# Optimization experiments

Hardware: AMD Instinct MI355X
Metric: run time of the kernel (lower is better)

The kernel has to match this reference:

```python
import jax, jax.numpy as jnp
import numpy as np

D_MODEL = 1024
D_FF = 4096
N_EXPERTS = 8
TOP_K = 2
BATCH, SEQ = 4, 1024


def setup_inputs() -> dict:
    key = jax.random.key(0)
    ks = jax.random.split(key, 5)
    x = jax.random.normal(ks[0], (BATCH, SEQ, D_MODEL), jnp.float32)
    Wr = jax.random.normal(ks[1], (D_MODEL, N_EXPERTS), jnp.float32) * (D_MODEL ** -0.5)
    W1 = jax.random.normal(ks[2], (N_EXPERTS, D_MODEL, D_FF), jnp.float32) * (D_MODEL ** -0.5)
    b1 = jnp.zeros((N_EXPERTS, D_FF), jnp.float32)
    W2 = jax.random.normal(ks[3], (N_EXPERTS, D_FF, D_MODEL), jnp.float32) * (D_FF ** -0.5)
    b2 = jnp.zeros((N_EXPERTS, D_MODEL), jnp.float32)
    return {"x": x, "Wr": Wr, "W1": W1, "b1": b1, "W2": W2, "b2": b2}


def reference(x, Wr, W1, b1, W2, b2):
    B, S, D = x.shape
    E = Wr.shape[1]
    xf = x.reshape(-1, D)                         # [T, D], T = B*S
    # Router: softmax over experts, pick top-k, renormalize gates over the k picks
    probs = jax.nn.softmax(xf @ Wr, axis=-1)      # [T, E]
    top_v, top_i = jax.lax.top_k(probs, TOP_K)    # [T, K]
    gates = top_v / jnp.sum(top_v, axis=-1, keepdims=True)
    # Combine weights per (token, expert): weight is gate if expert selected else 0
    cw = jnp.sum(gates[:, :, None] * jax.nn.one_hot(top_i, E, dtype=x.dtype), axis=1)  # [T, E]
    # Expert MLPs: loop over the small fixed expert count, weighted scatter-add combine
    out = jnp.zeros_like(xf)
    for e in range(E):
        h = jax.nn.relu(xf @ W1[e] + b1[e])       # [T, d_ff]
        y = h @ W2[e] + b2[e]                     # [T, D]
        out = out + cw[:, e:e + 1] * y
    return out.reshape(x.shape)
```

## Files before the change

kernel.cpp:

```cpp
#include <hip/hip_runtime.h>


#define T_TOK 4096
#define DMODEL 1024
#define DFF 4096
#define NE 8
#define CAP 9216

typedef __bf16 bf16x8 __attribute__((ext_vector_type(8)));
typedef float f32x4 __attribute__((ext_vector_type(4)));

__device__ __forceinline__ unsigned short f2bf(float f) {
    union { float f; unsigned u; } v; v.f = f;
    unsigned r = v.u + 0x7fffu + ((v.u >> 16) & 1u);
    return (unsigned short)(r >> 16);
}

__device__ __forceinline__ void gld16(const unsigned short* g, unsigned short* l) {
    __builtin_amdgcn_global_load_lds(
        (const __attribute__((address_space(1))) unsigned int*)g,
        (__attribute__((address_space(3))) unsigned int*)l, 16, 0, 0);
}

__global__ __launch_bounds__(256) void k_router(const float* __restrict__ x,
                                                const float* __restrict__ Wr,
                                                int* __restrict__ meta,
                                                int* __restrict__ tg_idx,
                                                float* __restrict__ tg_gate) {
    int wave = threadIdx.x >> 6, lane = threadIdx.x & 63;
    int t = blockIdx.x * 4 + wave;
    double acc[NE];
#pragma unroll
    for (int e = 0; e < NE; e++) acc[e] = 0.0;
    const float* xr = x + (size_t)t * DMODEL;
#pragma unroll 4
    for (int j = 0; j < 16; j++) {
        int k = j * 64 + lane;
        double xv = (double)xr[k];
        const float4* wr = (const float4*)(Wr + k * NE);
        float4 w0 = wr[0], w1 = wr[1];
        acc[0] += xv * (double)w0.x; acc[1] += xv * (double)w0.y;
        acc[2] += xv * (double)w0.z; acc[3] += xv * (double)w0.w;
        acc[4] += xv * (double)w1.x; acc[5] += xv * (double)w1.y;
        acc[6] += xv * (double)w1.z; acc[7] += xv * (double)w1.w;
    }
#pragma unroll
    for (int off = 32; off; off >>= 1)
#pragma unroll
        for (int e = 0; e < NE; e++) acc[e] += __shfl_xor(acc[e], off);
    if (lane == 0) {
        double v1 = -1e300, v2 = -1e300; int i1 = 0, i2 = 0;
#pragma unroll
        for (int e = 0; e < NE; e++) {
            double v = acc[e];
            if (v > v1) { v2 = v1; i2 = i1; v1 = v; i1 = e; }
            else if (v > v2) { v2 = v; i2 = e; }
        }
        double g1 = 1.0 / (1.0 + exp(v2 - v1));
        tg_idx[t * 2] = i1; tg_idx[t * 2 + 1] = i2;
        tg_gate[t * 2] = (float)g1; tg_gate[t * 2 + 1] = (float)(1.0 - g1);
        atomicAdd(&meta[i1], 1);
        atomicAdd(&meta[i2], 1);
    }
}

__global__ void k_scan(int* __restrict__ meta) {
    if (threadIdx.x == 0) {
        int acc = 0;
        for (int e = 0; e < NE; e++) {
            int a = (meta[e] + 127) & ~127;
            meta[16 + e] = a;
            meta[24 + e] = acc;
            acc += a;
        }
        meta[24 + NE] = acc;
        meta[33] = acc;
    }
}

__global__ __launch_bounds__(256) void k_build(const int* __restrict__ tg_idx,
                                               const float* __restrict__ tg_gate,
                                               int* __restrict__ meta,
                                               int* __restrict__ tos,
                                               float* __restrict__ gos,
                                               int* __restrict__ sot) {
    int t = blockIdx.x * 256 + threadIdx.x;
#pragma unroll
    for (int kk = 0; kk < 2; kk++) {
        int e = tg_idx[t * 2 + kk];
        int pos = atomicAdd(&meta[8 + e], 1);
        int slot = meta[24 + e] + pos;
        tos[slot] = t;
        gos[slot] = tg_gate[t * 2 + kk];
        sot[t * 2 + kk] = slot;
    }
}

__global__ __launch_bounds__(256) void k_gather(const float* __restrict__ x,
                                                const int* __restrict__ tos,
                                                const int* __restrict__ meta,
                                                unsigned short* __restrict__ xg) {
    int s = blockIdx.x;
    if (s >= meta[33]) return;
    int t = tos[s];
    int tid = threadIdx.x;
#pragma unroll
    for (int j = 0; j < 4; j++) {
        int k = tid + j * 256;
        float v = (t >= 0) ? x[(size_t)t * DMODEL + k] : 0.f;
        xg[(size_t)s * DMODEL + k] = f2bf(v);
    }
}

__global__ __launch_bounds__(256) void k_transpose2(const float* __restrict__ W1,
                                                    unsigned short* __restrict__ W1t,
                                                    const float* __restrict__ W2,
                                                    unsigned short* __restrict__ W2t) {
    int id = blockIdx.x;
    const float* in; unsigned short* out; int R, C, rem;
    if (id < 4096) { in = W1; out = W1t; R = DMODEL; C = DFF; rem = id; }
    else           { in = W2; out = W2t; R = DFF; C = DMODEL; rem = id - 4096; }
    int e = rem >> 9, r2 = rem & 511;
    int nbx = C >> 7;
    int bx = r2 % nbx, by = r2 / nbx;
    const float* src = in + (size_t)e * R * C;
    unsigned short* dst = out + (size_t)e * R * C;
    int g = threadIdx.x >> 3, l8 = threadIdx.x & 7;
    int rb = by * 64 + l8 * 8;
    int cb = bx * 128 + g * 4;
    f32x4 v[8];
#pragma unroll
    for (int i = 0; i < 8; i++)
        v[i] = *(const f32x4*)&src[(size_t)(rb + i) * C + cb];
#pragma unroll
    for (int j = 0; j < 4; j++) {
        unsigned short o[8];
#pragma unroll
        for (int i = 0; i < 8; i++) o[i] = f2bf(v[i][j]);
        *(uint4*)&dst[(size_t)(cb + j) * R + rb] = *(uint4*)o;
    }
}

template <int MODE>
__global__ __launch_bounds__(256, 4) void k_gemm(const unsigned short* __restrict__ A,
                                                 const unsigned short* __restrict__ Bt,
                                                 const float* __restrict__ bias,
                                                 const int* __restrict__ meta,
                                                 unsigned short* __restrict__ H,
                                                 float* __restrict__ Y) {
    constexpr int KFULL = (MODE == 1) ? DMODEL : DFF;
    constexpr int K     = (MODE == 1) ? DMODEL : DFF / 2;
    constexpr int N     = (MODE == 1) ? DFF : DMODEL;
    constexpr int TPM   = (MODE == 1) ? (DFF / 128) : (DMODEL / 128) * 2;

    int rem = blockIdx.x;
    int e = -1;
#pragma unroll
    for (int ee = 0; ee < NE; ee++) {
        if (e < 0) {
            int te = (meta[16 + ee] >> 7) * TPM;
            if (rem < te) e = ee; else rem -= te;
        }
    }
    if (e < 0) return;
    int mt = rem / TPM;
    int sub = rem - mt * TPM;
    int nt, kq;
    if constexpr (MODE == 1) { nt = sub; kq = 0; }
    else                     { kq = sub >> 3; nt = sub & 7; }
    int row0 = meta[24 + e] + mt * 128;
    int col0 = nt * 128;
    const unsigned short* Ae = A + (size_t)row0 * KFULL + kq * K;
    const unsigned short* Be = Bt + (size_t)e * N * KFULL + (size_t)col0 * KFULL + kq * K;
    const float* be = bias + (size_t)e * N;

    __shared__ __align__(16) unsigned short As[128 * 64];
    __shared__ __align__(16) unsigned short Bs[128 * 64];

    int tid = threadIdx.x;
    int lane = tid & 63, wave = tid >> 6;
    int wy = wave >> 1, wx = wave & 1;
    int q = lane >> 4, r16 = lane & 15;

    int srow = lane >> 3;
    int schunk = (lane & 7) ^ srow;
    int sgoff = srow * KFULL + schunk * 8;

    f32x4 acc[4][4];
#pragma unroll
    for (int i = 0; i < 4; i++)
#pragma unroll
        for (int j = 0; j < 4; j++) acc[i][j] = (f32x4){0.f, 0.f, 0.f, 0.f};

    for (int k0 = 0; k0 < K; k0 += 64) {
        __syncthreads();
#pragma unroll
        for (int it = 0; it < 4; it++) {
            int gr = wave * 32 + it * 8;
            gld16(Ae + (size_t)gr * KFULL + k0 + sgoff, &As[gr * 64]);
            gld16(Be + (size_t)gr * KFULL + k0 + sgoff, &Bs[gr * 64]);
        }
        __syncthreads();
#pragma unroll
        for (int ks = 0; ks < 2; ks++) {
            bf16x8 af[4], bfr[4];
            int sw = (r16 & 7);
#pragma unroll
            for (int i = 0; i < 4; i++) {
                int m = wy * 64 + i * 16 + r16;
                af[i] = *(const bf16x8*)&As[m * 64 + (((ks * 4 + q) ^ sw) << 3)];
            }
#pragma unroll
            for (int j = 0; j < 4; j++) {
                int n = wx * 64 + j * 16 + r16;
                bfr[j] = *(const bf16x8*)&Bs[n * 64 + (((ks * 4 + q) ^ sw) << 3)];
            }
#pragma unroll
            for (int i = 0; i < 4; i++)
#pragma unroll
                for (int j = 0; j < 4; j++)
                    acc[i][j] = __builtin_amdgcn_mfma_f32_16x16x32_bf16(af[i], bfr[j], acc[i][j], 0, 0, 0);
        }
    }

    if constexpr (MODE == 1) {
#pragma unroll
        for (int i = 0; i < 4; i++) {
#pragma unroll
            for (int rr = 0; rr < 4; rr++) {
                int gs = row0 + wy * 64 + i * 16 + q * 4 + rr;
#pragma unroll
                for (int j = 0; j < 4; j++) {
                    int gn = col0 + wx * 64 + j * 16 + r16;
                    float v = acc[i][j][rr] + be[gn];
                    H[(size_t)gs * DFF + gn] = f2bf(v > 0.f ? v : 0.f);
                }
            }
        }
    } else {
        float* Yp = Y + (size_t)kq * CAP * DMODEL;
#pragma unroll
        for (int i = 0; i < 4; i++) {
#pragma unroll
            for (int rr = 0; rr < 4; rr++) {
                int gs = row0 + wy * 64 + i * 16 + q * 4 + rr;
#pragma unroll
                for (int j = 0; j < 4; j++) {
                    int gn = col0 + wx * 64 + j * 16 + r16;
                    Yp[(size_t)gs * DMODEL + gn] = acc[i][j][rr];
                }
            }
        }
    }
}

__global__ __launch_bounds__(256) void k_combine(const float* __restrict__ Y,
                                                 const int* __restrict__ tg_idx,
                                                 const float* __restrict__ tg_gate,
                                                 const int* __restrict__ sot,
                                                 const float* __restrict__ b2,
                                                 float* __restrict__ out) {
    int t = blockIdx.x;
    int e0 = tg_idx[t * 2], e1 = tg_idx[t * 2 + 1];
    float g0 = tg_gate[t * 2], g1 = tg_gate[t * 2 + 1];
    int s0 = sot[t * 2], s1 = sot[t * 2 + 1];
    const float* y0 = Y;
    const float* y1 = Y + (size_t)CAP * DMODEL;
    int d = threadIdx.x * 4;
    f32x4 a0 = *(const f32x4*)&y0[(size_t)s0 * DMODEL + d];
    f32x4 b0 = *(const f32x4*)&y1[(size_t)s0 * DMODEL + d];
    f32x4 a1 = *(const f32x4*)&y0[(size_t)s1 * DMODEL + d];
    f32x4 b1v = *(const f32x4*)&y1[(size_t)s1 * DMODEL + d];
    f32x4 c0 = *(const f32x4*)&b2[(size_t)e0 * DMODEL + d];
    f32x4 c1 = *(const f32x4*)&b2[(size_t)e1 * DMODEL + d];
    f32x4 r;
#pragma unroll
    for (int i = 0; i < 4; i++)
        r[i] = g0 * (a0[i] + b0[i] + c0[i]) + g1 * (a1[i] + b1v[i] + c1[i]);
    *(f32x4*)&out[(size_t)t * DMODEL + d] = r;
}

extern "C" void kernel_launch(void* const* d_in, const int* in_sizes, int n_in,
                              void* d_out, int out_size, void* d_ws, size_t ws_size,
                              hipStream_t stream) {
    const float* x  = (const float*)d_in[0];
    const float* Wr = (const float*)d_in[1];
    const float* W1 = (const float*)d_in[2];
    const float* b1 = (const float*)d_in[3];
    const float* W2 = (const float*)d_in[4];
    const float* b2 = (const float*)d_in[5];
    float* out = (float*)d_out;

    char* p = (char*)d_ws;
    auto alloc = [&](size_t bytes) {
        char* q = p;
        p += (bytes + 255) & ~(size_t)255;
        return q;
    };
    int*   meta    = (int*)alloc(64 * 4);
    int*   tg_idx  = (int*)alloc((size_t)T_TOK * 2 * 4);
    float* tg_gate = (float*)alloc((size_t)T_TOK * 2 * 4);
    int*   tos     = (int*)alloc((size_t)CAP * 4);
    float* gos     = (float*)alloc((size_t)CAP * 4);
    int*   sot     = (int*)alloc((size_t)T_TOK * 2 * 4);
    unsigned short* xg  = (unsigned short*)alloc((size_t)CAP * DMODEL * 2);
    unsigned short* W1t = (unsigned short*)alloc((size_t)NE * DMODEL * DFF * 2);
    unsigned short* W2t = (unsigned short*)alloc((size_t)NE * DMODEL * DFF * 2);
    unsigned short* h   = (unsigned short*)alloc((size_t)CAP * DFF * 2);
    float* y = (float*)xg;

    hipMemsetAsync(meta, 0, 64 * 4, stream);
    hipMemsetAsync(tos, 0xFF, (size_t)CAP * 4, stream);

    k_router<<<T_TOK / 4, 256, 0, stream>>>(x, Wr, meta, tg_idx, tg_gate);
    k_scan<<<1, 64, 0, stream>>>(meta);
    k_build<<<T_TOK / 256, 256, 0, stream>>>(tg_idx, tg_gate, meta, tos, gos, sot);
    k_gather<<<CAP, 256, 0, stream>>>(x, tos, meta, xg);
    k_transpose2<<<8192, 256, 0, stream>>>(W1, W1t, W2, W2t);
    k_gemm<1><<<dim3(72 * (DFF / 128)), 256, 0, stream>>>(xg, W1t, b1, meta, h, nullptr);
    k_gemm<2><<<dim3(72 * (DMODEL / 128) * 2), 256, 0, stream>>>(h, W2t, b2, meta, nullptr, y);
    k_combine<<<T_TOK, 256, 0, stream>>>(y, tg_idx, tg_gate, sot, b2, out);
}
```

Before: 688.1 us.

## Replace atomic routing count, scan and build kernels with one pack kernel

Routing metadata is now built by a single per-expert block kernel instead of global atomics in the router, a one-thread scan kernel, an atomic slot-build kernel and two memsets. Each block counts tokens per expert using packed 16-bit counters and a shared-memory tree reduction. It then computes expert offsets, runs a prefix scan to get per-thread write positions, and writes slots in token order, padding with -1 only up to its expert's aligned end. This removes launches, memsets and atomic contention, and makes slot order deterministic. In exchange every block rescans the full index array, and only eight blocks do the work.

```diff
diff --git a/kernel.cpp b/kernel.cpp
--- a/kernel.cpp
+++ b/kernel.cpp
@@ -24,7 +24,6 @@
 
 __global__ __launch_bounds__(256) void k_router(const float* __restrict__ x,
                                                 const float* __restrict__ Wr,
-                                                int* __restrict__ meta,
                                                 int* __restrict__ tg_idx,
                                                 float* __restrict__ tg_gate) {
     int wave = threadIdx.x >> 6, lane = threadIdx.x & 63;
@@ -59,40 +58,74 @@
         double g1 = 1.0 / (1.0 + exp(v2 - v1));
         tg_idx[t * 2] = i1; tg_idx[t * 2 + 1] = i2;
         tg_gate[t * 2] = (float)g1; tg_gate[t * 2 + 1] = (float)(1.0 - g1);
-        atomicAdd(&meta[i1], 1);
-        atomicAdd(&meta[i2], 1);
-    }
-}
-
-__global__ void k_scan(int* __restrict__ meta) {
-    if (threadIdx.x == 0) {
-        int acc = 0;
-        for (int e = 0; e < NE; e++) {
-            int a = (meta[e] + 127) & ~127;
-            meta[16 + e] = a;
-            meta[24 + e] = acc;
-            acc += a;
-        }
-        meta[24 + NE] = acc;
-        meta[33] = acc;
-    }
-}
-
-__global__ __launch_bounds__(256) void k_build(const int* __restrict__ tg_idx,
-                                               const float* __restrict__ tg_gate,
-                                               int* __restrict__ meta,
-                                               int* __restrict__ tos,
-                                               float* __restrict__ gos,
-                                               int* __restrict__ sot) {
-    int t = blockIdx.x * 256 + threadIdx.x;
-#pragma unroll
-    for (int kk = 0; kk < 2; kk++) {
-        int e = tg_idx[t * 2 + kk];
-        int pos = atomicAdd(&meta[8 + e], 1);
-        int slot = meta[24 + e] + pos;
-        tos[slot] = t;
-        gos[slot] = tg_gate[t * 2 + kk];
-        sot[t * 2 + kk] = slot;
+    }
+}
+
+__global__ __launch_bounds__(256) void k_pack(const int* __restrict__ tg_idx,
+                                              int* __restrict__ meta,
+                                              int* __restrict__ tos,
+                                              int* __restrict__ sot) {
+    const int e = (int)blockIdx.x;
+    const int tid = (int)threadIdx.x;
+    const int CHUNK = (T_TOK * 2) / 256;
+    __shared__ unsigned long long slo[256];
+    __shared__ unsigned long long shi[256];
+    __shared__ int tsum[256];
+
+    int base = tid * CHUNK;
+    unsigned long long lo = 0, hi = 0;
+    int my = 0;
+    for (int i = 0; i < CHUNK; i++) {
+        int v = tg_idx[base + i];
+        unsigned long long inc = 1ull << ((v & 3) * 16);
+        if (v < 4) lo += inc; else hi += inc;
+        my += (v == e) ? 1 : 0;
+    }
+    slo[tid] = lo; shi[tid] = hi; tsum[tid] = my;
+    __syncthreads();
+    for (int off = 128; off > 0; off >>= 1) {
+        if (tid < off) {
+            slo[tid] += slo[tid + off];
+            shi[tid] += shi[tid + off];
+        }
+        __syncthreads();
+    }
+    unsigned long long tlo = slo[0], thi = shi[0];
+    int cnt[NE];
+#pragma unroll
+    for (int k = 0; k < 4; k++) {
+        cnt[k]     = (int)((tlo >> (k * 16)) & 0xffffu);
+        cnt[k + 4] = (int)((thi >> (k * 16)) & 0xffffu);
+    }
+    int off_e = 0, tot = 0;
+#pragma unroll
+    for (int k = 0; k < NE; k++) {
+        int a = (cnt[k] + 127) & ~127;
+        if (k < e) off_e += a;
+        tot += a;
+    }
+    int cnt_e = cnt[e];
+    int aligned_e = (cnt_e + 127) & ~127;
+    for (int off = 1; off < 256; off <<= 1) {
+        int v = (tid >= off) ? tsum[tid - off] : 0;
+        __syncthreads();
+        tsum[tid] += v;
+        __syncthreads();
+    }
+    int w = off_e + tsum[tid] - my;
+    for (int i = 0; i < CHUNK; i++) {
+        int idx = base + i;
+        if (tg_idx[idx] == e) {
+            tos[w] = idx >> 1;
+            sot[idx] = w;
+            w++;
+        }
+    }
+    for (int i = cnt_e + tid; i < aligned_e; i += 256) tos[off_e + i] = -1;
+    if (tid == 0) {
+        meta[16 + e] = aligned_e;
+        meta[24 + e] = off_e;
+        if (e == 0) meta[33] = tot;
     }
 }
 
@@ -301,7 +334,6 @@
     int*   tg_idx  = (int*)alloc((size_t)T_TOK * 2 * 4);
     float* tg_gate = (float*)alloc((size_t)T_TOK * 2 * 4);
     int*   tos     = (int*)alloc((size_t)CAP * 4);
-    float* gos     = (float*)alloc((size_t)CAP * 4);
     int*   sot     = (int*)alloc((size_t)T_TOK * 2 * 4);
     unsigned short* xg  = (unsigned short*)alloc((size_t)CAP * DMODEL * 2);
     unsigned short* W1t = (unsigned short*)alloc((size_t)NE * DMODEL * DFF * 2);
@@ -309,12 +341,8 @@
     unsigned short* h   = (unsigned short*)alloc((size_t)CAP * DFF * 2);
     float* y = (float*)xg;
 
-    hipMemsetAsync(meta, 0, 64 * 4, stream);
-    hipMemsetAsync(tos, 0xFF, (size_t)CAP * 4, stream);
-
-    k_router<<<T_TOK / 4, 256, 0, stream>>>(x, Wr, meta, tg_idx, tg_gate);
-    k_scan<<<1, 64, 0, stream>>>(meta);
-    k_build<<<T_TOK / 256, 256, 0, stream>>>(tg_idx, tg_gate, meta, tos, gos, sot);
+    k_router<<<T_TOK / 4, 256, 0, stream>>>(x, Wr, tg_idx, tg_gate);
+    k_pack<<<NE, 256, 0, stream>>>(tg_idx, meta, tos, sot);
     k_gather<<<CAP, 256, 0, stream>>>(x, tos, meta, xg);
     k_transpose2<<<8192, 256, 0, stream>>>(W1, W1t, W2, W2t);
     k_gemm<1><<<dim3(72 * (DFF / 128)), 256, 0, stream>>>(xg, W1t, b1, meta, h, nullptr);
```

New measurement: 554.8 us. -19.4%, faster.
